# Optimization experiments

Hardware: AMD Instinct MI355X
Metric: run time of the kernel (lower is better)

The kernel has to match this reference:

```python
import jax, jax.numpy as jnp
import numpy as np

DIM = 256
NUM_HEADS = 4
HEAD_DIM = DIM // NUM_HEADS
SCALE = HEAD_DIM ** -0.5
LOGIT_CLAMP = 6.0


def _conv1x1(x, w, b):
    # x: (B,C,H,W), w: (Cout,Cin), b: (Cout,)
    return jnp.einsum('bchw,oc->bohw', x, w) + b[None, :, None, None]


def setup_inputs() -> dict:
    key = jax.random.key(0)
    ks = jax.random.split(key, 10)
    B, C, H, W = 8, DIM, 48, 48
    init = lambda k, shape, fan_in: jax.random.normal(k, shape, jnp.float32) * (fan_in ** -0.5)
    return {
        'src_feat': jax.random.normal(ks[0], (B, C, H, W), jnp.float32),
        'tgt_feat': jax.random.normal(ks[1], (B, C, H, W), jnp.float32),
        'qw': init(ks[2], (DIM, DIM), DIM), 'qb': jnp.zeros((DIM,), jnp.float32),
        'kw': init(ks[3], (DIM, DIM), DIM), 'kb': jnp.zeros((DIM,), jnp.float32),
        'vw': init(ks[4], (DIM, DIM), DIM), 'vb': jnp.zeros((DIM,), jnp.float32),
        'ow': init(ks[5], (DIM, DIM), DIM), 'ob': jnp.zeros((DIM,), jnp.float32),
    }


def reference(src_feat, tgt_feat, qw, qb, kw, kb, vw, vb, ow, ob):
    B, C, H, W = src_feat.shape
    N = H * W
    Q = _conv1x1(src_feat, qw, qb)
    K = _conv1x1(tgt_feat, kw, kb)
    V = _conv1x1(tgt_feat, vw, vb)
    # (B,C,H,W) -> (B,heads,head_dim,N) -> (B,heads,N,head_dim)
    to_heads = lambda t: t.reshape(B, NUM_HEADS, HEAD_DIM, N).transpose(0, 1, 3, 2)
    Qh, Kh, Vh = to_heads(Q), to_heads(K), to_heads(V)
    attn = jnp.einsum('bhnd,bhmd->bhnm', Qh, Kh) * SCALE
    attn = jnp.clip(attn, -LOGIT_CLAMP, LOGIT_CLAMP)
    attn = jax.nn.softmax(attn, axis=-1)
    out = jnp.einsum('bhnm,bhmd->bhnd', attn, Vh)
    out = out.transpose(0, 1, 3, 2).reshape(B, C, H, W)
    return _conv1x1(out, ow, ob)
```

## Files before the change

kernel.cpp:

```cpp
#include <hip/hip_runtime.h>
#include <hip/hip_bf16.h>

#define DIM 256
#define NHEADS 4
#define HDIM 64
#define NPIX 2304
#define NBATCH 8
#define KCN 72
#define NTN 144
#define SCALE_L2E 0.18033688011112042f
#define CLAMP_L2E 8.656170245332781f

typedef __hip_bfloat16 bf16;
typedef __bf16 bf16x8 __attribute__((ext_vector_type(8)));
typedef float  f32x4  __attribute__((ext_vector_type(4)));
typedef float  f32x16 __attribute__((ext_vector_type(16)));

__device__ __forceinline__ unsigned int pack2bf(float a, float b) {
    __hip_bfloat162 h = __float22bfloat162_rn(float2{a, b});
    union { __hip_bfloat162 h; unsigned int u; } c; c.h = h;
    return c.u;
}

__global__ __launch_bounds__(256) void cvt_w_kernel(
    const float* __restrict__ w0, const float* __restrict__ w1,
    const float* __restrict__ w2, const float* __restrict__ w3,
    bf16* __restrict__ out)
{
    const int sel = blockIdx.y;
    const float* src = sel == 0 ? w0 : sel == 1 ? w1 : sel == 2 ? w2 : w3;
    const int i = blockIdx.x * 256 + threadIdx.x;
    const int m = i >> 5, c0 = (i & 31) * 8;
    const int mh = m >> 7, mt = (m >> 4) & 7, lo = m & 15;
    const int kc = c0 >> 5, hi = (c0 >> 3) & 3;
    float4 a = *(const float4*)(src + i * 8);
    float4 b = *(const float4*)(src + i * 8 + 4);
    uint4 u;
    u.x = pack2bf(a.x, a.y); u.y = pack2bf(a.z, a.w);
    u.z = pack2bf(b.x, b.y); u.w = pack2bf(b.z, b.w);
    const size_t fb = (((size_t)(mh * 8 + kc)) * 8 + mt) * 512 + (hi * 16 + lo) * 8;
    *(uint4*)(void*)(out + (size_t)sel * 65536 + fb) = u;
}

__global__ __launch_bounds__(256) void txp_kernel(
    const float* __restrict__ src, const float* __restrict__ tgt,
    bf16* __restrict__ oS, bf16* __restrict__ oT)
{
    const int b = blockIdx.z & 7;
    const float* in = (blockIdx.z >> 3) ? tgt : src;
    bf16* out = (blockIdx.z >> 3) ? oT : oS;
    const int n0 = blockIdx.x * 64, c0 = blockIdx.y * 64;
    __shared__ float tile[64][65];
    const int t = threadIdx.x;
#pragma unroll
    for (int i = 0; i < 4; ++i) {
        int idx = t + i * 256;
        int cl = idx >> 4, n4 = (idx & 15) * 4;
        float4 v = *(const float4*)(in + ((size_t)b * DIM + c0 + cl) * NPIX + n0 + n4);
        tile[cl][n4] = v.x; tile[cl][n4 + 1] = v.y;
        tile[cl][n4 + 2] = v.z; tile[cl][n4 + 3] = v.w;
    }
    __syncthreads();
#pragma unroll
    for (int i = 0; i < 2; ++i) {
        int idx = t + i * 256;
        int nl = idx >> 3, c8 = (idx & 7) * 8;
        uint4 u;
        u.x = pack2bf(tile[c8 + 0][nl], tile[c8 + 1][nl]);
        u.y = pack2bf(tile[c8 + 2][nl], tile[c8 + 3][nl]);
        u.z = pack2bf(tile[c8 + 4][nl], tile[c8 + 5][nl]);
        u.w = pack2bf(tile[c8 + 6][nl], tile[c8 + 7][nl]);
        const int n = n0 + nl, c = c0 + c8;
        const size_t fb = (((size_t)(b * NTN + (n >> 4))) * 8 + (c >> 5)) * 512
                        + ((((c >> 3) & 3) * 16) + (n & 15)) * 8;
        *(uint4*)(void*)(out + fb) = u;
    }
}

__device__ __forceinline__ void conv_core(
    const bf16* __restrict__ xp, const bf16* __restrict__ wp,
    int wk, f32x4 (&acc)[8])
{
#pragma unroll
    for (int mt = 0; mt < 8; ++mt) acc[mt] = (f32x4){0.f, 0.f, 0.f, 0.f};

    const int kbase = wk * 4;
    bf16x8 a = *(const bf16x8*)(const void*)(xp + (size_t)kbase * 512);
    bf16x8 bfr[8];
#pragma unroll
    for (int mt = 0; mt < 8; ++mt)
        bfr[mt] = *(const bf16x8*)(const void*)(wp + (size_t)(kbase * 8 + mt) * 512);

#pragma unroll
    for (int ki = 0; ki < 4; ++ki) {
        const int kn = kbase + ((ki + 1) & 3);
        bf16x8 a2 = *(const bf16x8*)(const void*)(xp + (size_t)kn * 512);
        bf16x8 bfr2[8];
#pragma unroll
        for (int mt = 0; mt < 8; ++mt)
            bfr2[mt] = *(const bf16x8*)(const void*)(wp + (size_t)(kn * 8 + mt) * 512);
#pragma unroll
        for (int mt = 0; mt < 8; ++mt)
            acc[mt] = __builtin_amdgcn_mfma_f32_16x16x32_bf16(a, bfr[mt], acc[mt], 0, 0, 0);
        a = a2;
#pragma unroll
        for (int mt = 0; mt < 8; ++mt) bfr[mt] = bfr2[mt];
    }
}

__global__ __launch_bounds__(256, 3) void conv_qkv_kernel(
    const bf16* __restrict__ XS, const bf16* __restrict__ XT,
    const bf16* __restrict__ Wbf,
    const float* __restrict__ qb, const float* __restrict__ kb2,
    const float* __restrict__ vb2,
    bf16* __restrict__ Qt, bf16* __restrict__ Kt, bf16* __restrict__ Vt)
{
    const int b  = blockIdx.z;
    const int sel = blockIdx.y >> 1, mh = blockIdx.y & 1;
    const int n0 = blockIdx.x * 32;
    const int w  = threadIdx.x >> 6, l = threadIdx.x & 63;
    const int wn = w & 1, wk = w >> 1;
    const int lo = l & 15, hi = l >> 4;

    __shared__ float red[2][64][36];

    const bf16* X = sel == 0 ? XS : XT;
    const float* bias = sel == 0 ? qb : sel == 1 ? kb2 : vb2;
    const float scale = sel == 0 ? SCALE_L2E : 1.0f;
    bf16* Yb = sel == 0 ? Qt : sel == 1 ? Kt : Vt;

    const int ntile = blockIdx.x * 2 + wn;
    const bf16* xp = X + ((size_t)(b * NTN + ntile) * 8) * 512 + l * 8;
    const bf16* wp = Wbf + (size_t)sel * 65536 + (size_t)mh * 32768 + l * 8;

    f32x4 acc[8];
    conv_core(xp, wp, wk, acc);

    if (wk == 1) {
#pragma unroll
        for (int mt = 0; mt < 8; ++mt)
            *(float4*)&red[wn][l][mt * 4] = make_float4(acc[mt][0], acc[mt][1],
                                                        acc[mt][2], acc[mt][3]);
    }
    __syncthreads();
    if (wk != 0) return;

#pragma unroll
    for (int mt = 0; mt < 8; ++mt) {
        float4 v = *(float4*)&red[wn][l][mt * 4];
        acc[mt][0] += v.x; acc[mt][1] += v.y; acc[mt][2] += v.z; acc[mt][3] += v.w;
    }

    const int nb = n0 + wn * 16 + hi * 4;
#pragma unroll
    for (int mt = 0; mt < 8; ++mt) {
        const int m = mh * 128 + mt * 16 + lo;
        const float bv = bias[m];
        if (sel < 2) {
            const int h = m >> 6, d = m & 63;
            const size_t fb = (((size_t)(b * NHEADS + h) * KCN + (nb >> 5)) * 4 + (d >> 4)) * 512
                            + ((((d >> 3) & 1) * 32) + (nb & 31)) * 8 + (d & 7);
#pragma unroll
            for (int r = 0; r < 4; ++r)
                Yb[fb + r * 8] = __float2bfloat16((acc[mt][r] + bv) * scale);
        } else {
            const int h = m >> 6, dv = m & 63;
            const size_t fb = ((((size_t)(b * NHEADS + h) * KCN + (nb >> 5)) * 2 + ((nb >> 4) & 1)) * 2
                               + (dv >> 5)) * 512
                            + ((((nb >> 3) & 1) * 32) + (dv & 31)) * 8 + (nb & 7);
            uint2 u = make_uint2(pack2bf(acc[mt][0] + bv, acc[mt][1] + bv),
                                 pack2bf(acc[mt][2] + bv, acc[mt][3] + bv));
            *(uint2*)(void*)(Yb + fb) = u;
        }
    }
}

__global__ __launch_bounds__(256, 3) void conv_out_kernel(
    const bf16* __restrict__ X, const bf16* __restrict__ Wb,
    const float* __restrict__ bias, float* __restrict__ Yf)
{
    const int b  = blockIdx.z, mh = blockIdx.y;
    const int n0 = blockIdx.x * 32;
    const int w  = threadIdx.x >> 6, l = threadIdx.x & 63;
    const int wn = w & 1, wk = w >> 1;
    const int lo = l & 15, hi = l >> 4;

    __shared__ float red[2][64][36];

    const int ntile = blockIdx.x * 2 + wn;
    const bf16* xp = X + ((size_t)(b * NTN + ntile) * 8) * 512 + l * 8;
    const bf16* wp = Wb + (size_t)mh * 32768 + l * 8;

    f32x4 acc[8];
    conv_core(xp, wp, wk, acc);

    if (wk == 1) {
#pragma unroll
        for (int mt = 0; mt < 8; ++mt)
            *(float4*)&red[wn][l][mt * 4] = make_float4(acc[mt][0], acc[mt][1],
                                                        acc[mt][2], acc[mt][3]);
    }
    __syncthreads();
    if (wk != 0) return;

#pragma unroll
    for (int mt = 0; mt < 8; ++mt) {
        float4 v = *(float4*)&red[wn][l][mt * 4];
        acc[mt][0] += v.x; acc[mt][1] += v.y; acc[mt][2] += v.z; acc[mt][3] += v.w;
    }

    const int nb = n0 + wn * 16 + hi * 4;
#pragma unroll
    for (int mt = 0; mt < 8; ++mt) {
        const int m = mh * 128 + mt * 16 + lo;
        const float bv = bias[m];
        float4 v = make_float4(acc[mt][0] + bv, acc[mt][1] + bv,
                               acc[mt][2] + bv, acc[mt][3] + bv);
        *(float4*)(void*)(Yf + ((size_t)b * DIM + m) * NPIX + nb) = v;
    }
}

__global__ __launch_bounds__(256, 3) void attn_kernel(
    const bf16* __restrict__ Qt, const bf16* __restrict__ Kt,
    const bf16* __restrict__ Vt, bf16* __restrict__ Op)
{
    const int b = blockIdx.z, h = blockIdx.y;
    const int w = threadIdx.x >> 6;
    const int wq = w & 1, wk = w >> 1;
    const int l = threadIdx.x & 63;
    const int ln = l & 31, h2 = l >> 5;
    const int bh = b * NHEADS + h;

    __shared__ float red[2][32][68];
    __shared__ float lred[2][32];

    const bf16* QB = Qt + ((size_t)bh * KCN + blockIdx.x * 2 + wq) * 2048 + l * 8;
    const bf16* KB = Kt + (size_t)bh * KCN * 2048 + l * 8;
    const bf16* VB = Vt + (size_t)bh * KCN * 2048 + l * 8;

    bf16x8 qf[4];
#pragma unroll
    for (int dk = 0; dk < 4; ++dk)
        qf[dk] = *(const bf16x8*)(const void*)(QB + dk * 512);

    f32x16 oacc[2];
#pragma unroll
    for (int dt = 0; dt < 2; ++dt)
#pragma unroll
        for (int r = 0; r < 16; ++r) oacc[dt][r] = 0.f;
    float lsum = 0.f;

    bf16x8 kfA[4], kfB[4];
    bf16x8 vfA[2][2], vfB[2][2];

    auto load_chunk = [&](int kc_, bf16x8 (&kfD)[4], bf16x8 (&vfD)[2][2]) {
        const bf16* KBn = KB + (size_t)kc_ * 2048;
        const bf16* VBn = VB + (size_t)kc_ * 2048;
#pragma unroll
        for (int dk = 0; dk < 4; ++dk)
            kfD[dk] = *(const bf16x8*)(const void*)(KBn + dk * 512);
#pragma unroll
        for (int kb = 0; kb < 2; ++kb)
#pragma unroll
            for (int dt = 0; dt < 2; ++dt)
                vfD[kb][dt] = *(const bf16x8*)(const void*)(VBn + kb * 1024 + dt * 512);
    };

    auto compute = [&](const bf16x8 (&kfX)[4], const bf16x8 (&vfX)[2][2]) {
        f32x16 s;
#pragma unroll
        for (int r = 0; r < 16; ++r) s[r] = 0.f;
#pragma unroll
        for (int dk = 0; dk < 4; ++dk)
            s = __builtin_amdgcn_mfma_f32_32x32x16_bf16(kfX[dk], qf[dk], s, 0, 0, 0);

        float ls = 0.f;
        unsigned int pk[8];
#pragma unroll
        for (int p = 0; p < 8; ++p) {
            float ea = __builtin_amdgcn_exp2f(
                __builtin_amdgcn_fmed3f(s[2 * p],     -CLAMP_L2E, CLAMP_L2E));
            float eb = __builtin_amdgcn_exp2f(
                __builtin_amdgcn_fmed3f(s[2 * p + 1], -CLAMP_L2E, CLAMP_L2E));
            ls += ea + eb;
            pk[p] = pack2bf(ea, eb);
        }
        lsum += ls;

        unsigned int c00 = pk[0], c02 = pk[2], c01 = pk[1], c03 = pk[3];
        unsigned int c10 = pk[4], c12 = pk[6], c11 = pk[5], c13 = pk[7];
        asm("v_permlane32_swap_b32 %0, %1" : "+v"(c00), "+v"(c02));
        asm("v_permlane32_swap_b32 %0, %1" : "+v"(c01), "+v"(c03));
        asm("v_permlane32_swap_b32 %0, %1" : "+v"(c10), "+v"(c12));
        asm("v_permlane32_swap_b32 %0, %1" : "+v"(c11), "+v"(c13));
        union { unsigned int u[4]; bf16x8 v; } pb0, pb1;
        pb0.u[0] = c00; pb0.u[1] = c01; pb0.u[2] = c02; pb0.u[3] = c03;
        pb1.u[0] = c10; pb1.u[1] = c11; pb1.u[2] = c12; pb1.u[3] = c13;

#pragma unroll
        for (int dt = 0; dt < 2; ++dt) {
            oacc[dt] = __builtin_amdgcn_mfma_f32_32x32x16_bf16(vfX[0][dt], pb0.v, oacc[dt], 0, 0, 0);
            oacc[dt] = __builtin_amdgcn_mfma_f32_32x32x16_bf16(vfX[1][dt], pb1.v, oacc[dt], 0, 0, 0);
        }
    };

    load_chunk(wk, kfA, vfA);
    for (int i = 0; i < 36; i += 2) {
        load_chunk(wk + 2 * (i + 1), kfB, vfB);
        compute(kfA, vfA);
        load_chunk(i + 2 < 36 ? wk + 2 * (i + 2) : wk, kfA, vfA);
        compute(kfB, vfB);
    }

    lsum += __shfl_xor(lsum, 32);
    if (wk == 1) {
        if (h2 == 0) lred[wq][ln] = lsum;
#pragma unroll
        for (int dt = 0; dt < 2; ++dt)
#pragma unroll
            for (int g = 0; g < 4; ++g) {
                float4 v = make_float4(oacc[dt][g * 4 + 0], oacc[dt][g * 4 + 1],
                                       oacc[dt][g * 4 + 2], oacc[dt][g * 4 + 3]);
                *(float4*)&red[wq][ln][dt * 32 + g * 8 + h2 * 4] = v;
            }
    }
    __syncthreads();

    if (wk == 0) {
#pragma unroll
        for (int dt = 0; dt < 2; ++dt)
#pragma unroll
            for (int g = 0; g < 4; ++g) {
                float4 v = *(float4*)&red[wq][ln][dt * 32 + g * 8 + h2 * 4];
                oacc[dt][g * 4 + 0] += v.x; oacc[dt][g * 4 + 1] += v.y;
                oacc[dt][g * 4 + 2] += v.z; oacc[dt][g * 4 + 3] += v.w;
            }
        const float inv = 1.f / (lsum + lred[wq][ln]);

        const int ntile = blockIdx.x * 4 + wq * 2 + (ln >> 4);
        bf16* opb = Op + (((size_t)(b * NTN + ntile)) * 8 + h * 2) * 512
                  + (ln & 15) * 8 + h2 * 4;
#pragma unroll
        for (int dt = 0; dt < 2; ++dt)
#pragma unroll
            for (int g = 0; g < 4; ++g) {
                float v0 = oacc[dt][g * 4 + 0] * inv;
                float v1 = oacc[dt][g * 4 + 1] * inv;
                float v2 = oacc[dt][g * 4 + 2] * inv;
                float v3 = oacc[dt][g * 4 + 3] * inv;
                uint2 u = make_uint2(pack2bf(v0, v1), pack2bf(v2, v3));
                *(uint2*)(void*)(opb + (size_t)dt * 512 + g * 128) = u;
            }
    }
}

extern "C" void kernel_launch(void* const* d_in, const int* in_sizes, int n_in,
                              void* d_out, int out_size, void* d_ws, size_t ws_size,
                              hipStream_t stream) {
    const float* src = (const float*)d_in[0];
    const float* tgt = (const float*)d_in[1];
    const float* qw  = (const float*)d_in[2];
    const float* qb  = (const float*)d_in[3];
    const float* kw  = (const float*)d_in[4];
    const float* kb  = (const float*)d_in[5];
    const float* vw  = (const float*)d_in[6];
    const float* vb  = (const float*)d_in[7];
    const float* ow  = (const float*)d_in[8];
    const float* ob  = (const float*)d_in[9];
    float* out = (float*)d_out;

    const size_t TEN = (size_t)NBATCH * DIM * NPIX;
    bf16* Wbf  = (bf16*)d_ws;
    bf16* XbfS = Wbf  + 4 * 65536;
    bf16* XbfT = XbfS + TEN;
    bf16* Qt   = XbfT + TEN;
    bf16* Kt   = Qt   + TEN;
    bf16* Vt   = Kt   + TEN;
    bf16* Op   = Vt   + TEN;

    cvt_w_kernel<<<dim3(32, 4, 1), 256, 0, stream>>>(qw, kw, vw, ow, Wbf);
    txp_kernel<<<dim3(NPIX / 64, DIM / 64, 2 * NBATCH), 256, 0, stream>>>(src, tgt, XbfS, XbfT);

    conv_qkv_kernel<<<dim3(NPIX / 32, 6, NBATCH), 256, 0, stream>>>(
        XbfS, XbfT, Wbf, qb, kb, vb, Qt, Kt, Vt);

    attn_kernel<<<dim3(NPIX / 64, NHEADS, NBATCH), 256, 0, stream>>>(Qt, Kt, Vt, Op);

    conv_out_kernel<<<dim3(NPIX / 32, 2, NBATCH), 256, 0, stream>>>(
        Op, Wbf + 3 * 65536, ob, out);
}
```

Baseline: 131.6 us.

## Process two query tiles per warp in attention to reuse K/V loads

Each warp in the attention kernel now handles two 32-row query sub-tiles instead of one, so every K/V fragment loaded from global memory feeds twice as many MFMAs. The grid is halved along the query axis and the launch-bounds occupancy hint drops from 3 to 2 blocks per CU to allow the extra accumulator and Q registers. The goal is to halve K/V global-memory traffic per unit of compute. The cost is more registers, lower occupancy, fewer blocks (576), and a doubled shared-memory reduction buffer.

After: 120.5 us. 1.09x faster.

```diff
diff --git a/kernel.cpp b/kernel.cpp
--- a/kernel.cpp
+++ b/kernel.cpp
@@ -220,7 +220,7 @@
     }
 }
 
-__global__ __launch_bounds__(256, 3) void attn_kernel(
+__global__ __launch_bounds__(256, 2) void attn_kernel(
     const bf16* __restrict__ Qt, const bf16* __restrict__ Kt,
     const bf16* __restrict__ Vt, bf16* __restrict__ Op)
 {
@@ -230,25 +230,30 @@
     const int l = threadIdx.x & 63;
     const int ln = l & 31, h2 = l >> 5;
     const int bh = b * NHEADS + h;
-
-    __shared__ float red[2][32][68];
-    __shared__ float lred[2][32];
-
-    const bf16* QB = Qt + ((size_t)bh * KCN + blockIdx.x * 2 + wq) * 2048 + l * 8;
+    const int qt = blockIdx.x;
+
+    __shared__ float red[2][2][32][68];
+    __shared__ float lred[2][2][32];
+
+    const bf16* QB = Qt + ((size_t)bh * KCN + qt * 4 + wq * 2) * 2048 + l * 8;
     const bf16* KB = Kt + (size_t)bh * KCN * 2048 + l * 8;
     const bf16* VB = Vt + (size_t)bh * KCN * 2048 + l * 8;
 
-    bf16x8 qf[4];
-#pragma unroll
-    for (int dk = 0; dk < 4; ++dk)
-        qf[dk] = *(const bf16x8*)(const void*)(QB + dk * 512);
-
-    f32x16 oacc[2];
-#pragma unroll
-    for (int dt = 0; dt < 2; ++dt)
-#pragma unroll
-        for (int r = 0; r < 16; ++r) oacc[dt][r] = 0.f;
-    float lsum = 0.f;
+    bf16x8 qf[2][4];
+#pragma unroll
+    for (int qs = 0; qs < 2; ++qs)
+#pragma unroll
+        for (int dk = 0; dk < 4; ++dk)
+            qf[qs][dk] = *(const bf16x8*)(const void*)(QB + qs * 2048 + dk * 512);
+
+    f32x16 oacc[2][2];
+#pragma unroll
+    for (int qs = 0; qs < 2; ++qs)
+#pragma unroll
+        for (int dt = 0; dt < 2; ++dt)
+#pragma unroll
+            for (int r = 0; r < 16; ++r) oacc[qs][dt][r] = 0.f;
+    float lsum[2] = {0.f, 0.f};
 
     bf16x8 kfA[4], kfB[4];
     bf16x8 vfA[2][2], vfB[2][2];
@@ -267,40 +272,43 @@
     };
 
     auto compute = [&](const bf16x8 (&kfX)[4], const bf16x8 (&vfX)[2][2]) {
-        f32x16 s;
-#pragma unroll
-        for (int r = 0; r < 16; ++r) s[r] = 0.f;
-#pragma unroll
-        for (int dk = 0; dk < 4; ++dk)
-            s = __builtin_amdgcn_mfma_f32_32x32x16_bf16(kfX[dk], qf[dk], s, 0, 0, 0);
-
-        float ls = 0.f;
-        unsigned int pk[8];
-#pragma unroll
-        for (int p = 0; p < 8; ++p) {
-            float ea = __builtin_amdgcn_exp2f(
-                __builtin_amdgcn_fmed3f(s[2 * p],     -CLAMP_L2E, CLAMP_L2E));
-            float eb = __builtin_amdgcn_exp2f(
-                __builtin_amdgcn_fmed3f(s[2 * p + 1], -CLAMP_L2E, CLAMP_L2E));
-            ls += ea + eb;
-            pk[p] = pack2bf(ea, eb);
-        }
-        lsum += ls;
-
-        unsigned int c00 = pk[0], c02 = pk[2], c01 = pk[1], c03 = pk[3];
-        unsigned int c10 = pk[4], c12 = pk[6], c11 = pk[5], c13 = pk[7];
-        asm("v_permlane32_swap_b32 %0, %1" : "+v"(c00), "+v"(c02));
-        asm("v_permlane32_swap_b32 %0, %1" : "+v"(c01), "+v"(c03));
-        asm("v_permlane32_swap_b32 %0, %1" : "+v"(c10), "+v"(c12));
-        asm("v_permlane32_swap_b32 %0, %1" : "+v"(c11), "+v"(c13));
-        union { unsigned int u[4]; bf16x8 v; } pb0, pb1;
-        pb0.u[0] = c00; pb0.u[1] = c01; pb0.u[2] = c02; pb0.u[3] = c03;
-        pb1.u[0] = c10; pb1.u[1] = c11; pb1.u[2] = c12; pb1.u[3] = c13;
-
-#pragma unroll
-        for (int dt = 0; dt < 2; ++dt) {
-            oacc[dt] = __builtin_amdgcn_mfma_f32_32x32x16_bf16(vfX[0][dt], pb0.v, oacc[dt], 0, 0, 0);
-            oacc[dt] = __builtin_amdgcn_mfma_f32_32x32x16_bf16(vfX[1][dt], pb1.v, oacc[dt], 0, 0, 0);
+#pragma unroll
+        for (int qs = 0; qs < 2; ++qs) {
+            f32x16 s;
+#pragma unroll
+            for (int r = 0; r < 16; ++r) s[r] = 0.f;
+#pragma unroll
+            for (int dk = 0; dk < 4; ++dk)
+                s = __builtin_amdgcn_mfma_f32_32x32x16_bf16(kfX[dk], qf[qs][dk], s, 0, 0, 0);
+
+            float ls = 0.f;
+            unsigned int pk[8];
+#pragma unroll
+            for (int p = 0; p < 8; ++p) {
+                float ea = __builtin_amdgcn_exp2f(
+                    __builtin_amdgcn_fmed3f(s[2 * p],     -CLAMP_L2E, CLAMP_L2E));
+                float eb = __builtin_amdgcn_exp2f(
+                    __builtin_amdgcn_fmed3f(s[2 * p + 1], -CLAMP_L2E, CLAMP_L2E));
+                ls += ea + eb;
+                pk[p] = pack2bf(ea, eb);
+            }
+            lsum[qs] += ls;
+
+            unsigned int c00 = pk[0], c02 = pk[2], c01 = pk[1], c03 = pk[3];
+            unsigned int c10 = pk[4], c12 = pk[6], c11 = pk[5], c13 = pk[7];
+            asm("v_permlane32_swap_b32 %0, %1" : "+v"(c00), "+v"(c02));
+            asm("v_permlane32_swap_b32 %0, %1" : "+v"(c01), "+v"(c03));
+            asm("v_permlane32_swap_b32 %0, %1" : "+v"(c10), "+v"(c12));
+            asm("v_permlane32_swap_b32 %0, %1" : "+v"(c11), "+v"(c13));
+            union { unsigned int u[4]; bf16x8 v; } pb0, pb1;
+            pb0.u[0] = c00; pb0.u[1] = c01; pb0.u[2] = c02; pb0.u[3] = c03;
+            pb1.u[0] = c10; pb1.u[1] = c11; pb1.u[2] = c12; pb1.u[3] = c13;
+
+#pragma unroll
+            for (int dt = 0; dt < 2; ++dt) {
+                oacc[qs][dt] = __builtin_amdgcn_mfma_f32_32x32x16_bf16(vfX[0][dt], pb0.v, oacc[qs][dt], 0, 0, 0);
+                oacc[qs][dt] = __builtin_amdgcn_mfma_f32_32x32x16_bf16(vfX[1][dt], pb1.v, oacc[qs][dt], 0, 0, 0);
+            }
         }
     };
 
@@ -312,45 +320,51 @@
         compute(kfB, vfB);
     }
 
-    lsum += __shfl_xor(lsum, 32);
+#pragma unroll
+    for (int qs = 0; qs < 2; ++qs) lsum[qs] += __shfl_xor(lsum[qs], 32);
     if (wk == 1) {
-        if (h2 == 0) lred[wq][ln] = lsum;
-#pragma unroll
-        for (int dt = 0; dt < 2; ++dt)
-#pragma unroll
-            for (int g = 0; g < 4; ++g) {
-                float4 v = make_float4(oacc[dt][g * 4 + 0], oacc[dt][g * 4 + 1],
-                                       oacc[dt][g * 4 + 2], oacc[dt][g * 4 + 3]);
-                *(float4*)&red[wq][ln][dt * 32 + g * 8 + h2 * 4] = v;
-            }
+        if (h2 == 0) { lred[wq][0][ln] = lsum[0]; lred[wq][1][ln] = lsum[1]; }
+#pragma unroll
+        for (int qs = 0; qs < 2; ++qs)
+#pragma unroll
+            for (int dt = 0; dt < 2; ++dt)
+#pragma unroll
+                for (int g = 0; g < 4; ++g) {
+                    float4 v = make_float4(oacc[qs][dt][g * 4 + 0], oacc[qs][dt][g * 4 + 1],
+                                           oacc[qs][dt][g * 4 + 2], oacc[qs][dt][g * 4 + 3]);
+                    *(float4*)&red[wq][qs][ln][dt * 32 + g * 8 + h2 * 4] = v;
+                }
     }
     __syncthreads();
 
     if (wk == 0) {
 #pragma unroll
-        for (int dt = 0; dt < 2; ++dt)
-#pragma unroll
-            for (int g = 0; g < 4; ++g) {
-                float4 v = *(float4*)&red[wq][ln][dt * 32 + g * 8 + h2 * 4];
-                oacc[dt][g * 4 + 0] += v.x; oacc[dt][g * 4 + 1] += v.y;
-                oacc[dt][g * 4 + 2] += v.z; oacc[dt][g * 4 + 3] += v.w;
-            }
-        const float inv = 1.f / (lsum + lred[wq][ln]);
-
-        const int ntile = blockIdx.x * 4 + wq * 2 + (ln >> 4);
-        bf16* opb = Op + (((size_t)(b * NTN + ntile)) * 8 + h * 2) * 512
-                  + (ln & 15) * 8 + h2 * 4;
-#pragma unroll
-        for (int dt = 0; dt < 2; ++dt)
-#pragma unroll
-            for (int g = 0; g < 4; ++g) {
-                float v0 = oacc[dt][g * 4 + 0] * inv;
-                float v1 = oacc[dt][g * 4 + 1] * inv;
-                float v2 = oacc[dt][g * 4 + 2] * inv;
-                float v3 = oacc[dt][g * 4 + 3] * inv;
-                uint2 u = make_uint2(pack2bf(v0, v1), pack2bf(v2, v3));
-                *(uint2*)(void*)(opb + (size_t)dt * 512 + g * 128) = u;
-            }
+        for (int qs = 0; qs < 2; ++qs) {
+#pragma unroll
+            for (int dt = 0; dt < 2; ++dt)
+#pragma unroll
+                for (int g = 0; g < 4; ++g) {
+                    float4 v = *(float4*)&red[wq][qs][ln][dt * 32 + g * 8 + h2 * 4];
+                    oacc[qs][dt][g * 4 + 0] += v.x; oacc[qs][dt][g * 4 + 1] += v.y;
+                    oacc[qs][dt][g * 4 + 2] += v.z; oacc[qs][dt][g * 4 + 3] += v.w;
+                }
+            const float inv = 1.f / (lsum[qs] + lred[wq][qs][ln]);
+
+            const int ntile = qt * 8 + wq * 4 + qs * 2 + (ln >> 4);
+            bf16* opb = Op + (((size_t)(b * NTN + ntile)) * 8 + h * 2) * 512
+                      + (ln & 15) * 8 + h2 * 4;
+#pragma unroll
+            for (int dt = 0; dt < 2; ++dt)
+#pragma unroll
+                for (int g = 0; g < 4; ++g) {
+                    float v0 = oacc[qs][dt][g * 4 + 0] * inv;
+                    float v1 = oacc[qs][dt][g * 4 + 1] * inv;
+                    float v2 = oacc[qs][dt][g * 4 + 2] * inv;
+                    float v3 = oacc[qs][dt][g * 4 + 3] * inv;
+                    uint2 u = make_uint2(pack2bf(v0, v1), pack2bf(v2, v3));
+                    *(uint2*)(void*)(opb + (size_t)dt * 512 + g * 128) = u;
+                }
+        }
     }
 }
 
@@ -384,7 +398,7 @@
     conv_qkv_kernel<<<dim3(NPIX / 32, 6, NBATCH), 256, 0, stream>>>(
         XbfS, XbfT, Wbf, qb, kb, vb, Qt, Kt, Vt);
 
-    attn_kernel<<<dim3(NPIX / 64, NHEADS, NBATCH), 256, 0, stream>>>(Qt, Kt, Vt, Op);
+    attn_kernel<<<dim3(NPIX / 128, NHEADS, NBATCH), 256, 0, stream>>>(Qt, Kt, Vt, Op);
 
     conv_out_kernel<<<dim3(NPIX / 32, 2, NBATCH), 256, 0, stream>>>(
         Op, Wbf + 3 * 65536, ob, out);
```
